# Optimization experiments

Hardware: AMD Instinct MI355X
Metric: run time of the kernel (lower is better)

The kernel has to match this reference:

```python
import jax, jax.numpy as jnp
import numpy as np

DIM = 256
D_STATE = 16
D_CONV = 4
EXPAND = 2
D_INNER = DIM * EXPAND          # 512
DT_RANK = DIM // 16             # 16


def _dwconv(x_bcl, w, b, pad):
    # depthwise 1d conv; x_bcl: (B, C, L), w: (C, 1, K)
    out = jax.lax.conv_general_dilated(
        x_bcl, w, window_strides=(1,), padding=[pad],
        feature_group_count=x_bcl.shape[1],
        dimension_numbers=('NCH', 'OIH', 'NCH'))
    return out + b[None, :, None]


def _forward(x, ln_w, ln_b, W_in, conv_w, conv_b, W_xproj, W_dt, b_dt,
             A_log, D_ssm, W_outp, c1_w, c1_b, c2_w, c2_b, c3_w, c3_b,
             W_out, b_out, W_skip, b_skip):
    Bsz, C = x.shape[:2]
    img_dims = x.shape[2:]
    L = int(np.prod(img_dims))
    xf = x.reshape(Bsz, C, L).transpose(0, 2, 1)          # (B, L, C)
    # LayerNorm over channel dim
    mu = jnp.mean(xf, axis=-1, keepdims=True)
    var = jnp.var(xf, axis=-1, keepdims=True)
    xn = (xf - mu) / jnp.sqrt(var + 1e-5) * ln_w + ln_b   # (B, L, C)

    # ---------------- Mamba block ----------------
    xz = xn @ W_in.T                                      # (B, L, 2*Di)
    xi, z = jnp.split(xz, 2, axis=-1)
    k = conv_w.shape[-1]
    # causal depthwise conv (pad left d_conv-1, truncate to L), then silu
    xc = _dwconv(xi.transpose(0, 2, 1), conv_w, conv_b, (k - 1, 0))
    xc = jax.nn.silu(xc).transpose(0, 2, 1)               # (B, L, Di)
    x_dbl = xc @ W_xproj.T                                # (B, L, dt_rank + 2*N)
    dt = x_dbl[..., :DT_RANK]
    B_s = x_dbl[..., DT_RANK:DT_RANK + D_STATE]           # (B, L, N)
    C_s = x_dbl[..., DT_RANK + D_STATE:]                  # (B, L, N)
    delta = jax.nn.softplus(dt @ W_dt.T + b_dt)           # (B, L, Di)
    A = -jnp.exp(A_log)                                   # (Di, N)
    dA = jnp.exp(delta[..., None] * A)                    # (B, L, Di, N)
    dBu = (delta * xc)[..., None] * B_s[:, :, None, :]    # (B, L, Di, N)

    def step(h, inp):
        dA_t, dBu_t, c_t = inp
        h = dA_t * h + dBu_t                              # (B, Di, N)
        y = jnp.einsum('bdn,bn->bd', h, c_t)
        return h, y

    h0 = jnp.zeros((Bsz, D_INNER, D_STATE), dtype=x.dtype)
    _, ys = jax.lax.scan(
        step, h0,
        (dA.transpose(1, 0, 2, 3), dBu.transpose(1, 0, 2, 3), C_s.transpose(1, 0, 2)))
    y = ys.transpose(1, 0, 2) + D_ssm * xc                # (B, L, Di)
    y = y * jax.nn.silu(z)
    x_ssm = y @ W_outp.T                                  # (B, L, C)

    # ---------------- multi-scale depthwise convs ----------------
    xnT = xn.transpose(0, 2, 1)                           # (B, C, L)

    def msconv(w, b):
        kk = w.shape[-1]
        return jax.nn.silu(_dwconv(xnT, w, b, (kk // 2, kk // 2))).transpose(0, 2, 1)

    combined = x_ssm + msconv(c1_w, c1_b) + msconv(c2_w, c2_b) + msconv(c3_w, c3_b)
    out = combined @ W_out.T + b_out + xn @ W_skip.T + b_skip
    out = out.transpose(0, 2, 1).reshape(x.shape)
    return out + x


def setup_inputs() -> dict:
    key = jax.random.key(0)
    ks = jax.random.split(key, 12)

    def rn(k, shape, s=0.02):
        return jax.random.normal(k, shape, dtype=jnp.float32) * s

    return {
        'x': jax.random.normal(ks[0], (2, DIM, 64, 64), dtype=jnp.float32),
        'ln_w': jnp.ones((DIM,), jnp.float32),
        'ln_b': jnp.zeros((DIM,), jnp.float32),
        'W_in': rn(ks[1], (2 * D_INNER, DIM)),
        'conv_w': rn(ks[2], (D_INNER, 1, D_CONV), 0.1),
        'conv_b': jnp.zeros((D_INNER,), jnp.float32),
        'W_xproj': rn(ks[3], (DT_RANK + 2 * D_STATE, D_INNER)),
        'W_dt': rn(ks[4], (D_INNER, DT_RANK), 0.1),
        'b_dt': jnp.full((D_INNER,), -4.0, jnp.float32),  # softplus(-4) ~ 0.018, stable dt
        'A_log': jnp.log(jnp.broadcast_to(
            jnp.arange(1, D_STATE + 1, dtype=jnp.float32), (D_INNER, D_STATE))),
        'D_ssm': jnp.ones((D_INNER,), jnp.float32),
        'W_outp': rn(ks[5], (DIM, D_INNER)),
        'c1_w': rn(ks[6], (DIM, 1, 3), 0.1),
        'c1_b': jnp.zeros((DIM,), jnp.float32),
        'c2_w': rn(ks[7], (DIM, 1, 5), 0.1),
        'c2_b': jnp.zeros((DIM,), jnp.float32),
        'c3_w': rn(ks[8], (DIM, 1, 7), 0.1),
        'c3_b': jnp.zeros((DIM,), jnp.float32),
        'W_out': rn(ks[9], (DIM, DIM)),
        'b_out': jnp.zeros((DIM,), jnp.float32),
        'W_skip': rn(ks[10], (DIM, DIM)),
        'b_skip': jnp.zeros((DIM,), jnp.float32),
    }


def reference(x, ln_w, ln_b, W_in, conv_w, conv_b, W_xproj, W_dt, b_dt,
              A_log, D_ssm, W_outp, c1_w, c1_b, c2_w, c2_b, c3_w, c3_b,
              W_out, b_out, W_skip, b_skip):
    return _forward(x, ln_w, ln_b, W_in, conv_w, conv_b, W_xproj, W_dt, b_dt,
                    A_log, D_ssm, W_outp, c1_w, c1_b, c2_w, c2_b, c3_w, c3_b,
                    W_out, b_out, W_skip, b_skip)
```

## Files before the change

### kernel.cpp

```cpp
#include <hip/hip_runtime.h>
#include <hip/hip_bf16.h>
#include <math.h>
#include <cstddef>

#define BSZ 2
#define DM 256
#define LSEQ 4096
#define DIN 512
#define DXZ 1024
#define DS 16
#define RANK 16
#define GXP 48
#define LC 16
#define NC 256
#define CSTRIDE (BSZ * DIN * 16)

typedef __attribute__((ext_vector_type(8))) short short8;
typedef __attribute__((ext_vector_type(4))) float f32x4;
struct bf4 { __hip_bfloat16 v[4]; };

__device__ __forceinline__ float silu_f(float x){ return x / (1.f + __expf(-x)); }
__device__ __forceinline__ float softplus_f(float x){ return fmaxf(x, 0.f) + log1pf(__expf(-fabsf(x))); }
__device__ __forceinline__ float b2f(__hip_bfloat16 v){ return __bfloat162float(v); }
__device__ __forceinline__ __hip_bfloat16 f2b(float v){ return __float2bfloat16(v); }

__device__ __forceinline__ void gl_lds16(const void* g, void* s){
    __builtin_amdgcn_global_load_lds((const __attribute__((address_space(1))) void*)g,
                                     (__attribute__((address_space(3))) void*)s, 16, 0, 0);
}

__global__ __launch_bounds__(256) void k_pre(const float* __restrict__ x,
                                             const float* __restrict__ lnw, const float* __restrict__ lnb,
                                             const float* __restrict__ W_in, const float* __restrict__ W_xproj,
                                             const float* __restrict__ W_outp, const float* __restrict__ W_out,
                                             const float* __restrict__ W_skip, const float* __restrict__ b_out,
                                             const float* __restrict__ b_skip, const float* __restrict__ W_dt,
                                             const float* __restrict__ c1w, const float* __restrict__ c1b,
                                             const float* __restrict__ c2w, const float* __restrict__ c2b,
                                             const float* __restrict__ c3w, const float* __restrict__ c3b,
                                             __hip_bfloat16* __restrict__ xnb,
                                             __hip_bfloat16* __restrict__ Winb, __hip_bfloat16* __restrict__ Wxpb,
                                             __hip_bfloat16* __restrict__ Wopb, __hip_bfloat16* __restrict__ Wcb,
                                             __hip_bfloat16* __restrict__ Wdtb, float* __restrict__ bc,
                                             float* __restrict__ msw){
    __shared__ float tile[DM * 33];
    __shared__ float rsum[8][32], rsq[8][32];
    __shared__ float mu_s[32], rs_s[32];
    int tid = threadIdx.x;
    if (blockIdx.x < 256){
        int b  = blockIdx.x >> 7;
        int l0 = (blockIdx.x & 127) << 5;
        const float* xb = x + (size_t)b * DM * LSEQ;
        int lls = tid & 31, chi = tid >> 5;
        for (int cc = 0; cc < 32; ++cc){
            int c = cc * 8 + chi;
            tile[c * 33 + lls] = xb[(size_t)c * LSEQ + l0 + lls];
        }
        __syncthreads();
        int part = tid >> 5, l = tid & 31;
        float s = 0.f, sq = 0.f;
        for (int i = 0; i < 32; ++i){
            float v = tile[(part * 32 + i) * 33 + l];
            s += v; sq += v * v;
        }
        rsum[part][l] = s; rsq[part][l] = sq;
        __syncthreads();
        if (tid < 32){
            float ts = 0.f, tq = 0.f;
            for (int p = 0; p < 8; ++p){ ts += rsum[p][tid]; tq += rsq[p][tid]; }
            float mu  = ts * (1.f / DM);
            float var = tq * (1.f / DM) - mu * mu;
            mu_s[tid] = mu;
            rs_s[tid] = rsqrtf(var + 1e-5f);
        }
        __syncthreads();
        int c0 = tid & 63, lh = tid >> 6;
        for (int i = 0; i < 8; ++i){
            int ll = lh + 4 * i;
            float mu = mu_s[ll], rs = rs_s[ll];
            __hip_bfloat16* orow = xnb + (size_t)(b * LSEQ + l0 + ll) * 512;
            for (int j = 0; j < 4; ++j){
                int c = c0 + 64 * j;
                orow[c] = f2b((tile[c * 33 + ll] - mu) * rs * lnw[c] + lnb[c]);
            }
        }
    } else {
        int i0 = (blockIdx.x - 256) * 256 + tid;
        const int T = 256 * 256;
        for (int j = i0; j < 1024 * 256; j += T) Winb[j] = f2b(W_in[j]);
        for (int j = i0; j < 64 * 512; j += T){
            int r = j >> 9;
            Wxpb[j] = f2b(r < GXP ? W_xproj[r * 512 + (j & 511)] : 0.f);
        }
        for (int j = i0; j < 256 * 512; j += T) Wopb[j] = f2b(W_outp[j]);
        for (int j = i0; j < 256 * 512; j += T){
            int n = j >> 9, k = j & 511;
            Wcb[j] = f2b(k < 256 ? W_out[n * 256 + k] : W_skip[n * 256 + (k - 256)]);
        }
        for (int j = i0; j < 512 * 32; j += T){
            int n = j >> 5, k = j & 31;
            Wdtb[j] = f2b(k < 16 ? W_dt[n * 16 + k] : 0.f);
        }
        if (i0 < 256){
            bc[i0] = b_out[i0] + b_skip[i0];
            float* m = msw + i0 * 20;
            m[0] = c1w[i0*3]; m[1] = c1w[i0*3+1]; m[2] = c1w[i0*3+2];
            for (int j = 0; j < 5; ++j) m[3+j] = c2w[i0*5+j];
            for (int j = 0; j < 7; ++j) m[8+j] = c3w[i0*7+j];
            m[15] = c1b[i0]; m[16] = c2b[i0]; m[17] = c3b[i0];
            m[18] = 0.f; m[19] = 0.f;
        }
    }
}

template<int EPI, int BM = 128, int BN = 64>
__global__ __launch_bounds__(256) void k_mgemm(const __hip_bfloat16* __restrict__ A, int lda,
                                               const __hip_bfloat16* __restrict__ W,
                                               const float* __restrict__ bias,
                                               void* __restrict__ Cv, int ldc,
                                               int N, int K,
                                               const float* __restrict__ xres = nullptr,
                                               const __hip_bfloat16* __restrict__ xnb2 = nullptr,
                                               const float* __restrict__ msw = nullptr){
    constexpr int SA  = BM / 8;
    constexpr int SAW = SA / 4;
    constexpr int SB  = BN / 8;
    constexpr int SBW = SB / 4;
    constexpr int WROWS = BM / 2;
    constexpr int WCOLS = BN / 2;
    constexpr int MI = WROWS / 16;
    constexpr int NI = WCOLS / 16;
    __shared__ __align__(16) __hip_bfloat16 As[BM * 64];
    __shared__ __align__(16) __hip_bfloat16 Ws[BN * 64];
    __shared__ float tileT[(EPI & 16) ? 64 * 65 : 1];
    const int tid = threadIdx.x;
    const int wave = tid >> 6, lane = tid & 63;
    const int brow = blockIdx.x * BM, bcol = blockIdx.y * BN;
    const int wm = wave >> 1, wn = wave & 1;

    const int a_row = lane >> 3;
    const int a_chk = lane & 7;
    const int a_scol = ((a_chk ^ a_row) * 8);

    const int lrow = lane & 15;
    const int kc = lane >> 4;
    const int r7 = lrow & 7;

    f32x4 acc[MI][NI] = {};

    for (int k0 = 0; k0 < K; k0 += 64){
#pragma unroll
        for (int j = 0; j < SAW; ++j){
            int seg = wave * SAW + j;
            const __hip_bfloat16* src = A + (size_t)(brow + seg * 8 + a_row) * lda + k0 + a_scol;
            gl_lds16(src, &As[seg * 512]);
        }
#pragma unroll
        for (int j = 0; j < SBW; ++j){
            int seg = wave * SBW + j;
            const __hip_bfloat16* src = W + (size_t)(bcol + seg * 8 + a_row) * K + k0 + a_scol;
            gl_lds16(src, &Ws[seg * 512]);
        }
        __syncthreads();
#pragma unroll
        for (int kk = 0; kk < 2; ++kk){
            int kchunk = kk * 4 + kc;
            short8 af[MI], bfr[NI];
#pragma unroll
            for (int mi = 0; mi < MI; ++mi){
                int row = wm * WROWS + mi * 16 + lrow;
                af[mi] = *(const short8*)&As[row * 64 + ((kchunk ^ r7) * 8)];
            }
#pragma unroll
            for (int ni = 0; ni < NI; ++ni){
                int row = wn * WCOLS + ni * 16 + lrow;
                bfr[ni] = *(const short8*)&Ws[row * 64 + ((kchunk ^ r7) * 8)];
            }
#pragma unroll
            for (int mi = 0; mi < MI; ++mi)
#pragma unroll
                for (int ni = 0; ni < NI; ++ni)
                    acc[mi][ni] = __builtin_amdgcn_mfma_f32_16x16x32_bf16(af[mi], bfr[ni], acc[mi][ni], 0, 0, 0);
        }
        __syncthreads();
    }

    if (EPI & 16){
#pragma unroll
        for (int ni = 0; ni < NI; ++ni){
            int nl = wn * WCOLS + ni * 16 + lrow;
#pragma unroll
            for (int mi = 0; mi < MI; ++mi){
                int ml = wm * WROWS + mi * 16 + kc * 4;
#pragma unroll
                for (int r = 0; r < 4; ++r)
                    tileT[nl * 65 + ml + r] = acc[mi][ni][r];
            }
        }
        __syncthreads();
        int b = brow >> 12, l0 = brow & 4095;
        int lr = tid & 63, nr = tid >> 6;
        float* out = (float*)Cv;
#pragma unroll
        for (int rr = 0; rr < 16; ++rr){
            int n = rr * 4 + nr;
            size_t o = (size_t)(b * DM + bcol + n) * LSEQ + l0 + lr;
            out[o] = tileT[n * 65 + lr] + bias[bcol + n] + xres[o];
        }
        return;
    }

    if (EPI & 32){
#pragma unroll
        for (int ni = 0; ni < NI; ++ni){
            int n = bcol + wn * WCOLS + ni * 16 + lrow;
            float4 wv0 = *(const float4*)&msw[n * 20];
            float4 wv1 = *(const float4*)&msw[n * 20 + 4];
            float4 wv2 = *(const float4*)&msw[n * 20 + 8];
            float4 wv3 = *(const float4*)&msw[n * 20 + 12];
            float4 wv4 = *(const float4*)&msw[n * 20 + 16];
#pragma unroll
            for (int mi = 0; mi < MI; ++mi){
                int m0 = brow + wm * WROWS + mi * 16 + kc * 4;
                int l  = m0 & (LSEQ - 1);
                int bL = m0 - l;
                float v[10];
#pragma unroll
                for (int k = 0; k < 10; ++k){
                    int ll = l - 3 + k;
                    v[k] = ((unsigned)ll < LSEQ) ? b2f(xnb2[(size_t)(bL + ll) * 512 + n]) : 0.f;
                }
#pragma unroll
                for (int r = 0; r < 4; ++r){
                    float a1 = wv3.w + wv0.x * v[r+2] + wv0.y * v[r+3] + wv0.z * v[r+4];
                    float a2 = wv4.x + wv0.w * v[r+1] + wv1.x * v[r+2] + wv1.y * v[r+3]
                                     + wv1.z * v[r+4] + wv1.w * v[r+5];
                    float a3 = wv4.y + wv2.x * v[r] + wv2.y * v[r+1] + wv2.z * v[r+2]
                                     + wv2.w * v[r+3] + wv3.x * v[r+4] + wv3.y * v[r+5]
                                     + wv3.z * v[r+6];
                    float res = acc[mi][ni][r] + silu_f(a1) + silu_f(a2) + silu_f(a3);
                    ((__hip_bfloat16*)Cv)[(size_t)(m0 + r) * ldc + n] = f2b(res);
                }
            }
        }
        return;
    }

#pragma unroll
    for (int ni = 0; ni < NI; ++ni){
        int n = bcol + wn * WCOLS + ni * 16 + lrow;
        if (n >= N) continue;
        float bv = (EPI & 1) ? bias[n] : 0.f;
#pragma unroll
        for (int mi = 0; mi < MI; ++mi){
            int m0 = brow + wm * WROWS + mi * 16 + kc * 4;
#pragma unroll
            for (int r = 0; r < 4; ++r){
                float v = acc[mi][ni][r] + bv;
                if (EPI & 8) ((__hip_bfloat16*)Cv)[(size_t)(m0 + r) * ldc + n] = f2b(v);
                else         ((float*)Cv)[(size_t)(m0 + r) * ldc + n] = v;
            }
        }
    }
}

__global__ __launch_bounds__(256) void k_xpdt(const __hip_bfloat16* __restrict__ A,
                                              const __hip_bfloat16* __restrict__ Wxp,
                                              const __hip_bfloat16* __restrict__ Wdt,
                                              const float* __restrict__ bdt,
                                              float* __restrict__ xdbl,
                                              __hip_bfloat16* __restrict__ delta){
    __shared__ __align__(16) __hip_bfloat16 As[32 * 64];
    __shared__ __align__(16) __hip_bfloat16 Ws[64 * 64];
    __shared__ __hip_bfloat16 xdl[32][34];
    const int tid = threadIdx.x, wave = tid >> 6, lane = tid & 63;
    const int brow = blockIdx.x * 32;
    const int wm = wave >> 1, wn = wave & 1;
    const int a_row = lane >> 3, a_chk = lane & 7, a_scol = ((a_chk ^ a_row) * 8);
    const int lrow = lane & 15, kc = lane >> 4, r7 = lrow & 7;

    for (int i = tid; i < 32 * 18; i += 256){
        int rr = i / 18, cc = 16 + i % 18;
        xdl[rr][cc] = f2b(0.f);
    }

    f32x4 acc[2] = {};
    for (int k0 = 0; k0 < 512; k0 += 64){
        {
            int seg = wave;
            gl_lds16(A + (size_t)(brow + seg * 8 + a_row) * 512 + k0 + a_scol, &As[seg * 512]);
        }
#pragma unroll
        for (int j = 0; j < 2; ++j){
            int seg = wave * 2 + j;
            gl_lds16(Wxp + (size_t)(seg * 8 + a_row) * 512 + k0 + a_scol, &Ws[seg * 512]);
        }
        __syncthreads();
#pragma unroll
        for (int kk = 0; kk < 2; ++kk){
            int kchunk = kk * 4 + kc;
            short8 af = *(const short8*)&As[(wm * 16 + lrow) * 64 + ((kchunk ^ r7) * 8)];
#pragma unroll
            for (int ni = 0; ni < 2; ++ni){
                short8 bfr = *(const short8*)&Ws[(wn * 32 + ni * 16 + lrow) * 64 + ((kchunk ^ r7) * 8)];
                acc[ni] = __builtin_amdgcn_mfma_f32_16x16x32_bf16(af, bfr, acc[ni], 0, 0, 0);
            }
        }
        __syncthreads();
    }

#pragma unroll
    for (int ni = 0; ni < 2; ++ni){
        int n = wn * 32 + ni * 16 + lrow;
        if (n < 48){
#pragma unroll
            for (int r = 0; r < 4; ++r){
                int ml = wm * 16 + kc * 4 + r;
                float fv = acc[ni][r];
                xdbl[(size_t)(brow + ml) * 48 + n] = fv;
                if (n < 16) xdl[ml][n] = f2b(fv);
            }
        }
    }
    __syncthreads();

#pragma unroll
    for (int ct8 = 0; ct8 < 8; ++ct8){
        int ct = wave * 8 + ct8;
        int n = ct * 16 + lrow;
        short8 bfr = *(const short8*)&Wdt[(size_t)n * 32 + kc * 8];
        float bv = bdt[n];
#pragma unroll
        for (int rt = 0; rt < 2; ++rt){
            short8 af = *(const short8*)&xdl[rt * 16 + lrow][kc * 8];
            f32x4 dacc = {};
            dacc = __builtin_amdgcn_mfma_f32_16x16x32_bf16(af, bfr, dacc, 0, 0, 0);
#pragma unroll
            for (int r = 0; r < 4; ++r){
                int m = brow + rt * 16 + kc * 4 + r;
                delta[(size_t)m * 512 + n] = f2b(softplus_f(dacc[r] + bv));
            }
        }
    }
}

__global__ __launch_bounds__(256) void k_conv(const __hip_bfloat16* __restrict__ xz,
                                              const float* __restrict__ cw,
                                              const float* __restrict__ cb,
                                              __hip_bfloat16* __restrict__ xc){
    int idx = blockIdx.x * 256 + threadIdx.x;
    int d4 = (idx & 127) * 4;
    int bl = idx >> 7;
    int l  = bl & (LSEQ - 1);
    const __hip_bfloat16* base = xz + (size_t)bl * DXZ + d4;
    float4 bias = *(const float4*)(cb + d4);
    float acc[4] = {bias.x, bias.y, bias.z, bias.w};
    float4 w0 = *(const float4*)(cw + (d4 + 0) * 4);
    float4 w1 = *(const float4*)(cw + (d4 + 1) * 4);
    float4 w2 = *(const float4*)(cw + (d4 + 2) * 4);
    float4 w3 = *(const float4*)(cw + (d4 + 3) * 4);
    const float* wj[4] = {(const float*)&w0, (const float*)&w1, (const float*)&w2, (const float*)&w3};
#pragma unroll
    for (int t = 0; t < 4; ++t){
        int ls = l - (3 - t);
        if (ls >= 0){
            bf4 v = *(const bf4*)(base - (size_t)(3 - t) * DXZ);
#pragma unroll
            for (int j = 0; j < 4; ++j) acc[j] += wj[j][t] * b2f(v.v[j]);
        }
    }
    bf4 o;
#pragma unroll
    for (int j = 0; j < 4; ++j) o.v[j] = f2b(silu_f(acc[j]));
    *(bf4*)(xc + (size_t)bl * DIN + d4) = o;
}

__global__ __launch_bounds__(512) void k_scan1(const __hip_bfloat16* __restrict__ delta,
                                               const __hip_bfloat16* __restrict__ xc,
                                               const float* __restrict__ xdbl,
                                               const float* __restrict__ A_log,
                                               float* __restrict__ Acar,
                                               float* __restrict__ Bcar){
    int bx = blockIdx.x;
    int dh = bx & 1;
    int c  = (bx >> 1) & (NC - 1);
    int b  = bx >> 9;
    int tid = threadIdx.x;
    int dloc = tid >> 1, nh = tid & 1;
    int d = dh * 256 + dloc;
    int n0 = nh * 8;
    int rb = b * LSEQ + c * LC;
    __shared__ __align__(16) __hip_bfloat16 dl[LC][256];
    __shared__ __align__(16) __hip_bfloat16 xl[LC][256];
    __shared__ float Bs[LC][DS];
    const int w = tid >> 6, lane = tid & 63;
    {
        size_t rowg = (size_t)(rb + 2 * w + (lane >> 5));
        int col = (lane & 31) * 8;
        gl_lds16(delta + rowg * 512 + dh * 256 + col, &dl[2 * w][0]);
        gl_lds16(xc    + rowg * 512 + dh * 256 + col, &xl[2 * w][0]);
    }
    if (tid < 256){
        int t = tid >> 4, n = tid & 15;
        Bs[t][n] = xdbl[(size_t)(rb + t) * GXP + RANK + n];
    }
    __syncthreads();
    float Av[8];
    float a1 = -__expf(A_log[d * 16]);
    bool fast = true;
#pragma unroll
    for (int j = 0; j < 8; ++j){
        Av[j] = -__expf(A_log[d * 16 + n0 + j]);
        fast = fast && (fabsf(Av[j] - (float)(n0 + j + 1) * a1) <= 1e-4f * fabsf(Av[j]) + 1e-7f);
    }
    float ap[8], ac[8];
#pragma unroll
    for (int j = 0; j < 8; ++j){ ap[j] = 1.f; ac[j] = 0.f; }
    if (fast){
#pragma unroll 4
        for (int t = 0; t < LC; ++t){
            float de = b2f(dl[t][dloc]);
            float u  = de * b2f(xl[t][dloc]);
            float p  = __expf(de * a1);
            float p2 = p * p, p3 = p2 * p, p4 = p2 * p2;
            float qda[8] = {p, p2, p3, p4, p4 * p, p4 * p2, p4 * p3, p4 * p4};
            float bp = nh ? qda[7] : 1.f;
#pragma unroll
            for (int j = 0; j < 8; ++j){
                float da = qda[j] * bp;
                ap[j] *= da;
                ac[j] = da * ac[j] + u * Bs[t][n0 + j];
            }
        }
    } else {
        for (int t = 0; t < LC; ++t){
            float de = b2f(dl[t][dloc]);
            float u  = de * b2f(xl[t][dloc]);
#pragma unroll
            for (int j = 0; j < 8; ++j){
                float da = __expf(de * Av[j]);
                ap[j] *= da;
                ac[j] = da * ac[j] + u * Bs[t][n0 + j];
            }
        }
    }
    size_t o = (size_t)c * CSTRIDE + (size_t)(b * DIN + d) * 16 + n0;
    *(float4*)(Acar + o)     = make_float4(ap[0], ap[1], ap[2], ap[3]);
    *(float4*)(Acar + o + 4) = make_float4(ap[4], ap[5], ap[6], ap[7]);
    *(float4*)(Bcar + o)     = make_float4(ac[0], ac[1], ac[2], ac[3]);
    *(float4*)(Bcar + o + 4) = make_float4(ac[4], ac[5], ac[6], ac[7]);
}

__global__ __launch_bounds__(256) void k_scan2(const float* __restrict__ Acar,
                                               const float* __restrict__ Bcar,
                                               float* __restrict__ hinit){
    __shared__ float a_s[16][257];
    __shared__ float b_s[16][257];
    const int tid = threadIdx.x;
    const int idx0 = blockIdx.x * 16;
    const int cs = tid >> 4, s_ld = tid & 15;
#pragma unroll
    for (int r = 0; r < 16; ++r){
        int c = r * 16 + cs;
        size_t g = (size_t)c * CSTRIDE + idx0 + s_ld;
        a_s[s_ld][c] = Acar[g];
        b_s[s_ld][c] = Bcar[g];
    }
    __syncthreads();
    const int lane = tid & 63, w = tid >> 6;
#pragma unroll
    for (int i = 0; i < 4; ++i){
        int s = w * 4 + i;
        float a4[4], b4[4];
#pragma unroll
        for (int k = 0; k < 4; ++k){ a4[k] = a_s[s][4 * lane + k]; b4[k] = b_s[s][4 * lane + k]; }
        float av = a4[0], bv = b4[0];
#pragma unroll
        for (int k = 1; k < 4; ++k){ bv = a4[k] * bv + b4[k]; av *= a4[k]; }
#pragma unroll
        for (int d2 = 1; d2 < 64; d2 <<= 1){
            float ao = __shfl_up(av, d2);
            float bo = __shfl_up(bv, d2);
            if (lane >= d2){ bv = av * bo + bv; av = ao * av; }
        }
        float bx = __shfl_up(bv, 1);
        if (lane == 0) bx = 0.f;
        float h = bx;
        b_s[s][4 * lane] = h;
#pragma unroll
        for (int k = 0; k < 3; ++k){ h = a4[k] * h + b4[k]; b_s[s][4 * lane + 1 + k] = h; }
    }
    __syncthreads();
#pragma unroll
    for (int r = 0; r < 16; ++r){
        int c = r * 16 + cs;
        hinit[(size_t)c * CSTRIDE + idx0 + s_ld] = b_s[s_ld][c];
    }
}

__global__ __launch_bounds__(512) void k_scan3(const __hip_bfloat16* __restrict__ delta,
                                               const __hip_bfloat16* __restrict__ xc,
                                               const __hip_bfloat16* __restrict__ xz,
                                               const float* __restrict__ xdbl,
                                               const float* __restrict__ A_log,
                                               const float* __restrict__ D_ssm,
                                               const float* __restrict__ hinit,
                                               __hip_bfloat16* __restrict__ y){
    int bx = blockIdx.x;
    int dh = bx & 1;
    int c  = (bx >> 1) & (NC - 1);
    int b  = bx >> 9;
    int tid = threadIdx.x;
    int dloc = tid >> 1, nh = tid & 1;
    int d = dh * 256 + dloc;
    int n0 = nh * 8;
    int rb = b * LSEQ + c * LC;
    __shared__ __align__(16) __hip_bfloat16 dl[LC][256];
    __shared__ __align__(16) __hip_bfloat16 xl[LC][256];
    __shared__ __align__(16) __hip_bfloat16 zl[LC][256];
    __shared__ float Bs[LC][DS], Cs[LC][DS];
    const int w = tid >> 6, lane = tid & 63;
    {
        size_t rowg = (size_t)(rb + 2 * w + (lane >> 5));
        int col = (lane & 31) * 8;
        gl_lds16(delta + rowg * 512 + dh * 256 + col, &dl[2 * w][0]);
        gl_lds16(xc    + rowg * 512 + dh * 256 + col, &xl[2 * w][0]);
        gl_lds16(xz    + rowg * 1024 + 512 + dh * 256 + col, &zl[2 * w][0]);
    }
    if (tid < 256){
        int t = tid >> 4, n = tid & 15;
        Bs[t][n] = xdbl[(size_t)(rb + t) * GXP + RANK + n];
    } else {
        int t = (tid >> 4) - 16, n = tid & 15;
        Cs[t][n] = xdbl[(size_t)(rb + t) * GXP + RANK + DS + n];
    }
    __syncthreads();
    float Av[8];
    float a1 = -__expf(A_log[d * 16]);
    bool fast = true;
#pragma unroll
    for (int j = 0; j < 8; ++j){
        Av[j] = -__expf(A_log[d * 16 + n0 + j]);
        fast = fast && (fabsf(Av[j] - (float)(n0 + j + 1) * a1) <= 1e-4f * fabsf(Av[j]) + 1e-7f);
    }
    float h[8];
    size_t ho = (size_t)c * CSTRIDE + (size_t)(b * DIN + d) * 16 + n0;
    {
        float4 h0 = *(const float4*)(hinit + ho);
        float4 h1 = *(const float4*)(hinit + ho + 4);
        h[0] = h0.x; h[1] = h0.y; h[2] = h0.z; h[3] = h0.w;
        h[4] = h1.x; h[5] = h1.y; h[6] = h1.z; h[7] = h1.w;
    }
    float Dd = D_ssm[d];
    if (fast){
#pragma unroll 4
        for (int t = 0; t < LC; ++t){
            float de  = b2f(dl[t][dloc]);
            float xcv = b2f(xl[t][dloc]);
            float u = de * xcv;
            float p  = __expf(de * a1);
            float p2 = p * p, p3 = p2 * p, p4 = p2 * p2;
            float qda[8] = {p, p2, p3, p4, p4 * p, p4 * p2, p4 * p3, p4 * p4};
            float bp = nh ? qda[7] : 1.f;
#pragma unroll
            for (int j = 0; j < 8; ++j)
                h[j] = (qda[j] * bp) * h[j] + u * Bs[t][n0 + j];
            float e0 = h[0] * Cs[t][n0]     + h[1] * Cs[t][n0 + 1];
            float e1 = h[2] * Cs[t][n0 + 2] + h[3] * Cs[t][n0 + 3];
            float e2 = h[4] * Cs[t][n0 + 4] + h[5] * Cs[t][n0 + 5];
            float e3 = h[6] * Cs[t][n0 + 6] + h[7] * Cs[t][n0 + 7];
            float yv = (e0 + e1) + (e2 + e3);
            yv += __shfl_xor(yv, 1);
            if (nh == 0){
                float zv = b2f(zl[t][dloc]);
                zl[t][dloc] = f2b((yv + Dd * xcv) * silu_f(zv));
            }
        }
    } else {
        for (int t = 0; t < LC; ++t){
            float de  = b2f(dl[t][dloc]);
            float xcv = b2f(xl[t][dloc]);
            float u = de * xcv;
            float yv = 0.f;
#pragma unroll
            for (int j = 0; j < 8; ++j){
                float da = __expf(de * Av[j]);
                h[j] = da * h[j] + u * Bs[t][n0 + j];
                yv += h[j] * Cs[t][n0 + j];
            }
            yv += __shfl_xor(yv, 1);
            if (nh == 0){
                float zv = b2f(zl[t][dloc]);
                zl[t][dloc] = f2b((yv + Dd * xcv) * silu_f(zv));
            }
        }
    }
    __syncthreads();
    {
        int row = tid >> 5, colv = (tid & 31) * 8;
        *(float4*)(y + (size_t)(rb + row) * 512 + dh * 256 + colv) = *(const float4*)(&zl[row][colv]);
    }
}

extern "C" void kernel_launch(void* const* d_in, const int* in_sizes, int n_in,
                              void* d_out, int out_size, void* d_ws, size_t ws_size,
                              hipStream_t stream){
    const float* x      = (const float*)d_in[0];
    const float* ln_w   = (const float*)d_in[1];
    const float* ln_b   = (const float*)d_in[2];
    const float* W_in   = (const float*)d_in[3];
    const float* conv_w = (const float*)d_in[4];
    const float* conv_b = (const float*)d_in[5];
    const float* W_xproj= (const float*)d_in[6];
    const float* W_dt   = (const float*)d_in[7];
    const float* b_dt   = (const float*)d_in[8];
    const float* A_log  = (const float*)d_in[9];
    const float* D_ssm  = (const float*)d_in[10];
    const float* W_outp = (const float*)d_in[11];
    const float* c1_w   = (const float*)d_in[12];
    const float* c1_b   = (const float*)d_in[13];
    const float* c2_w   = (const float*)d_in[14];
    const float* c2_b   = (const float*)d_in[15];
    const float* c3_w   = (const float*)d_in[16];
    const float* c3_b   = (const float*)d_in[17];
    const float* W_out  = (const float*)d_in[18];
    const float* b_out  = (const float*)d_in[19];
    const float* W_skip = (const float*)d_in[20];
    const float* b_skip = (const float*)d_in[21];
    float* out = (float*)d_out;

    char* base = (char*)d_ws;
    const size_t MB = 1024 * 1024;
    const size_t KB = 1024;
    __hip_bfloat16* Acomb = (__hip_bfloat16*)(base);
    __hip_bfloat16* xzb   = (__hip_bfloat16*)(base + 8*MB);
    __hip_bfloat16* xcb   = (__hip_bfloat16*)(base + 24*MB);
    float*          xdbl  = (float*)        (base + 32*MB);
    __hip_bfloat16* deltab= (__hip_bfloat16*)(base + 34*MB);
    float*          Acar  = (float*)        (base + 42*MB);
    float*          Bcar  = (float*)        (base + 58*MB);
    float*          hinit = (float*)        (base + 74*MB);
    __hip_bfloat16* Winb  = (__hip_bfloat16*)(base + 90*MB);
    __hip_bfloat16* Wxpb  = (__hip_bfloat16*)(base + 90*MB + 512*KB);
    __hip_bfloat16* Wopb  = (__hip_bfloat16*)(base + 90*MB + 576*KB);
    __hip_bfloat16* Wcb   = (__hip_bfloat16*)(base + 90*MB + 832*KB);
    __hip_bfloat16* Wdtb  = (__hip_bfloat16*)(base + 90*MB + 1088*KB);
    float*          bc    = (float*)        (base + 90*MB + 1120*KB);
    float*          msw   = (float*)        (base + 90*MB + 1124*KB);
    __hip_bfloat16* xnb   = Acomb + 256;
    __hip_bfloat16* ybf   = (__hip_bfloat16*)Bcar;

    const int M = BSZ * LSEQ;

    k_pre<<<dim3(512), dim3(256), 0, stream>>>(x, ln_w, ln_b, W_in, W_xproj, W_outp, W_out, W_skip,
                                               b_out, b_skip, W_dt, c1_w, c1_b, c2_w, c2_b, c3_w, c3_b,
                                               xnb, Winb, Wxpb, Wopb, Wcb, Wdtb, bc, msw);
    k_mgemm<8, 128, 128><<<dim3(64, 8), dim3(256), 0, stream>>>(xnb, 512, Winb, nullptr, xzb, DXZ, 1024, 256);
    k_conv<<<dim3(M * DIN / 4 / 256), dim3(256), 0, stream>>>(xzb, conv_w, conv_b, xcb);
    k_xpdt<<<dim3(256), dim3(256), 0, stream>>>(xcb, Wxpb, Wdtb, b_dt, xdbl, deltab);
    k_scan1<<<dim3(BSZ * NC * 2), dim3(512), 0, stream>>>(deltab, xcb, xdbl, A_log, Acar, Bcar);
    k_scan2<<<dim3(1024), dim3(256), 0, stream>>>(Acar, Bcar, hinit);
    k_scan3<<<dim3(BSZ * NC * 2), dim3(512), 0, stream>>>(deltab, xcb, xzb, xdbl, A_log, D_ssm, hinit, ybf);
    k_mgemm<32, 64, 64><<<dim3(128, 4), dim3(256), 0, stream>>>(ybf, 512, Wopb, nullptr, Acomb, 512, 256, 512,
                                                                nullptr, xnb, msw);
    k_mgemm<17, 64, 64><<<dim3(128, 4), dim3(256), 0, stream>>>(Acomb, 512, Wcb, bc, out, DM, 256, 512, x);
}
```

Baseline: 233.9 us.

## Fuse chunk-scan pass 1 into x-proj/delta kernel and store carries in bf16

```diff
diff --git a/kernel.cpp b/kernel.cpp
--- a/kernel.cpp
+++ b/kernel.cpp
@@ -268,11 +268,16 @@
                                               const __hip_bfloat16* __restrict__ Wxp,
                                               const __hip_bfloat16* __restrict__ Wdt,
                                               const float* __restrict__ bdt,
+                                              const float* __restrict__ A_log,
                                               float* __restrict__ xdbl,
-                                              __hip_bfloat16* __restrict__ delta){
+                                              __hip_bfloat16* __restrict__ delta,
+                                              __hip_bfloat16* __restrict__ Acar,
+                                              __hip_bfloat16* __restrict__ Bcar){
     __shared__ __align__(16) __hip_bfloat16 As[32 * 64];
     __shared__ __align__(16) __hip_bfloat16 Ws[64 * 64];
     __shared__ __hip_bfloat16 xdl[32][34];
+    __shared__ __hip_bfloat16 dls[32][520];
+    __shared__ float Bls[32][16];
     const int tid = threadIdx.x, wave = tid >> 6, lane = tid & 63;
     const int brow = blockIdx.x * 32;
     const int wm = wave >> 1, wn = wave & 1;
@@ -319,6 +324,7 @@
                 float fv = acc[ni][r];
                 xdbl[(size_t)(brow + ml) * 48 + n] = fv;
                 if (n < 16) xdl[ml][n] = f2b(fv);
+                else if (n < 32) Bls[ml][n - 16] = fv;
             }
         }
     }
@@ -337,9 +343,71 @@
             dacc = __builtin_amdgcn_mfma_f32_16x16x32_bf16(af, bfr, dacc, 0, 0, 0);
 #pragma unroll
             for (int r = 0; r < 4; ++r){
-                int m = brow + rt * 16 + kc * 4 + r;
-                delta[(size_t)m * 512 + n] = f2b(softplus_f(dacc[r] + bv));
-            }
+                int ml = rt * 16 + kc * 4 + r;
+                __hip_bfloat16 hv = f2b(softplus_f(dacc[r] + bv));
+                delta[(size_t)(brow + ml) * 512 + n] = hv;
+                dls[ml][n] = hv;
+            }
+        }
+    }
+    __syncthreads();
+
+    const int b = brow >> 12;
+    const int c0 = (brow & 4095) >> 4;
+#pragma unroll
+    for (int dd = 0; dd < 2; ++dd){
+        int d = dd * 256 + tid;
+        float a1 = -__expf(A_log[d * 16]);
+        float Av[16];
+        bool fast = true;
+#pragma unroll
+        for (int j = 0; j < 16; ++j){
+            Av[j] = -__expf(A_log[d * 16 + j]);
+            fast = fast && (fabsf(Av[j] - (float)(j + 1) * a1) <= 1e-4f * fabsf(Av[j]) + 1e-7f);
+        }
+#pragma unroll
+        for (int cc = 0; cc < 2; ++cc){
+            float ap[16], ac[16];
+#pragma unroll
+            for (int j = 0; j < 16; ++j){ ap[j] = 1.f; ac[j] = 0.f; }
+            if (fast){
+                for (int t = 0; t < LC; ++t){
+                    int ml = cc * 16 + t;
+                    float de = b2f(dls[ml][d]);
+                    float u  = de * b2f(A[(size_t)(brow + ml) * 512 + d]);
+                    float p  = __expf(de * a1);
+                    float q2 = p * p;
+                    float q3 = q2 * p, q4 = q2 * q2;
+                    float q5 = q4 * p, q6 = q4 * q2, q7 = q4 * q3, q8 = q4 * q4;
+                    float qa[16] = {p, q2, q3, q4, q5, q6, q7, q8,
+                                    q8 * p, q8 * q2, q8 * q3, q8 * q4, q8 * q5, q8 * q6, q8 * q7, q8 * q8};
+#pragma unroll
+                    for (int j = 0; j < 16; ++j){
+                        ap[j] *= qa[j];
+                        ac[j] = qa[j] * ac[j] + u * Bls[ml][j];
+                    }
+                }
+            } else {
+                for (int t = 0; t < LC; ++t){
+                    int ml = cc * 16 + t;
+                    float de = b2f(dls[ml][d]);
+                    float u  = de * b2f(A[(size_t)(brow + ml) * 512 + d]);
+#pragma unroll
+                    for (int j = 0; j < 16; ++j){
+                        float da = __expf(de * Av[j]);
+                        ap[j] *= da;
+                        ac[j] = da * ac[j] + u * Bls[ml][j];
+                    }
+                }
+            }
+            __hip_bfloat16 av16[16], bv16[16];
+#pragma unroll
+            for (int j = 0; j < 16; ++j){ av16[j] = f2b(ap[j]); bv16[j] = f2b(ac[j]); }
+            size_t o = (size_t)(c0 + cc) * CSTRIDE + (size_t)(b * DIN + d) * 16;
+            *(float4*)(Acar + o)     = *(const float4*)(av16);
+            *(float4*)(Acar + o + 8) = *(const float4*)(av16 + 8);
+            *(float4*)(Bcar + o)     = *(const float4*)(bv16);
+            *(float4*)(Bcar + o + 8) = *(const float4*)(bv16 + 8);
         }
     }
 }
@@ -375,85 +443,9 @@
     *(bf4*)(xc + (size_t)bl * DIN + d4) = o;
 }
 
-__global__ __launch_bounds__(512) void k_scan1(const __hip_bfloat16* __restrict__ delta,
-                                               const __hip_bfloat16* __restrict__ xc,
-                                               const float* __restrict__ xdbl,
-                                               const float* __restrict__ A_log,
-                                               float* __restrict__ Acar,
-                                               float* __restrict__ Bcar){
-    int bx = blockIdx.x;
-    int dh = bx & 1;
-    int c  = (bx >> 1) & (NC - 1);
-    int b  = bx >> 9;
-    int tid = threadIdx.x;
-    int dloc = tid >> 1, nh = tid & 1;
-    int d = dh * 256 + dloc;
-    int n0 = nh * 8;
-    int rb = b * LSEQ + c * LC;
-    __shared__ __align__(16) __hip_bfloat16 dl[LC][256];
-    __shared__ __align__(16) __hip_bfloat16 xl[LC][256];
-    __shared__ float Bs[LC][DS];
-    const int w = tid >> 6, lane = tid & 63;
-    {
-        size_t rowg = (size_t)(rb + 2 * w + (lane >> 5));
-        int col = (lane & 31) * 8;
-        gl_lds16(delta + rowg * 512 + dh * 256 + col, &dl[2 * w][0]);
-        gl_lds16(xc    + rowg * 512 + dh * 256 + col, &xl[2 * w][0]);
-    }
-    if (tid < 256){
-        int t = tid >> 4, n = tid & 15;
-        Bs[t][n] = xdbl[(size_t)(rb + t) * GXP + RANK + n];
-    }
-    __syncthreads();
-    float Av[8];
-    float a1 = -__expf(A_log[d * 16]);
-    bool fast = true;
-#pragma unroll
-    for (int j = 0; j < 8; ++j){
-        Av[j] = -__expf(A_log[d * 16 + n0 + j]);
-        fast = fast && (fabsf(Av[j] - (float)(n0 + j + 1) * a1) <= 1e-4f * fabsf(Av[j]) + 1e-7f);
-    }
-    float ap[8], ac[8];
-#pragma unroll
-    for (int j = 0; j < 8; ++j){ ap[j] = 1.f; ac[j] = 0.f; }
-    if (fast){
-#pragma unroll 4
-        for (int t = 0; t < LC; ++t){
-            float de = b2f(dl[t][dloc]);
-            float u  = de * b2f(xl[t][dloc]);
-            float p  = __expf(de * a1);
-            float p2 = p * p, p3 = p2 * p, p4 = p2 * p2;
-            float qda[8] = {p, p2, p3, p4, p4 * p, p4 * p2, p4 * p3, p4 * p4};
-            float bp = nh ? qda[7] : 1.f;
-#pragma unroll
-            for (int j = 0; j < 8; ++j){
-                float da = qda[j] * bp;
-                ap[j] *= da;
-                ac[j] = da * ac[j] + u * Bs[t][n0 + j];
-            }
-        }
-    } else {
-        for (int t = 0; t < LC; ++t){
-            float de = b2f(dl[t][dloc]);
-            float u  = de * b2f(xl[t][dloc]);
-#pragma unroll
-            for (int j = 0; j < 8; ++j){
-                float da = __expf(de * Av[j]);
-                ap[j] *= da;
-                ac[j] = da * ac[j] + u * Bs[t][n0 + j];
-            }
-        }
-    }
-    size_t o = (size_t)c * CSTRIDE + (size_t)(b * DIN + d) * 16 + n0;
-    *(float4*)(Acar + o)     = make_float4(ap[0], ap[1], ap[2], ap[3]);
-    *(float4*)(Acar + o + 4) = make_float4(ap[4], ap[5], ap[6], ap[7]);
-    *(float4*)(Bcar + o)     = make_float4(ac[0], ac[1], ac[2], ac[3]);
-    *(float4*)(Bcar + o + 4) = make_float4(ac[4], ac[5], ac[6], ac[7]);
-}
-
-__global__ __launch_bounds__(256) void k_scan2(const float* __restrict__ Acar,
-                                               const float* __restrict__ Bcar,
-                                               float* __restrict__ hinit){
+__global__ __launch_bounds__(256) void k_scan2(const __hip_bfloat16* __restrict__ Acar,
+                                               const __hip_bfloat16* __restrict__ Bcar,
+                                               __hip_bfloat16* __restrict__ hinit){
     __shared__ float a_s[16][257];
     __shared__ float b_s[16][257];
     const int tid = threadIdx.x;
@@ -463,8 +455,8 @@
     for (int r = 0; r < 16; ++r){
         int c = r * 16 + cs;
         size_t g = (size_t)c * CSTRIDE + idx0 + s_ld;
-        a_s[s_ld][c] = Acar[g];
-        b_s[s_ld][c] = Bcar[g];
+        a_s[s_ld][c] = b2f(Acar[g]);
+        b_s[s_ld][c] = b2f(Bcar[g]);
     }
     __syncthreads();
     const int lane = tid & 63, w = tid >> 6;
@@ -494,7 +486,7 @@
 #pragma unroll
     for (int r = 0; r < 16; ++r){
         int c = r * 16 + cs;
-        hinit[(size_t)c * CSTRIDE + idx0 + s_ld] = b_s[s_ld][c];
+        hinit[(size_t)c * CSTRIDE + idx0 + s_ld] = f2b(b_s[s_ld][c]);
     }
 }
 
@@ -504,7 +496,7 @@
                                                const float* __restrict__ xdbl,
                                                const float* __restrict__ A_log,
                                                const float* __restrict__ D_ssm,
-                                               const float* __restrict__ hinit,
+                                               const __hip_bfloat16* __restrict__ hinit,
                                                __hip_bfloat16* __restrict__ y){
     int bx = blockIdx.x;
     int dh = bx & 1;
@@ -546,10 +538,9 @@
     float h[8];
     size_t ho = (size_t)c * CSTRIDE + (size_t)(b * DIN + d) * 16 + n0;
     {
-        float4 h0 = *(const float4*)(hinit + ho);
-        float4 h1 = *(const float4*)(hinit + ho + 4);
-        h[0] = h0.x; h[1] = h0.y; h[2] = h0.z; h[3] = h0.w;
-        h[4] = h1.x; h[5] = h1.y; h[6] = h1.z; h[7] = h1.w;
+        short8 hv = *(const short8*)(hinit + ho);
+#pragma unroll
+        for (int j = 0; j < 8; ++j) h[j] = b2f(((const __hip_bfloat16*)&hv)[j]);
     }
     float Dd = D_ssm[d];
     if (fast){
@@ -637,18 +628,18 @@
     __hip_bfloat16* xcb   = (__hip_bfloat16*)(base + 24*MB);
     float*          xdbl  = (float*)        (base + 32*MB);
     __hip_bfloat16* deltab= (__hip_bfloat16*)(base + 34*MB);
-    float*          Acar  = (float*)        (base + 42*MB);
-    float*          Bcar  = (float*)        (base + 58*MB);
-    float*          hinit = (float*)        (base + 74*MB);
-    __hip_bfloat16* Winb  = (__hip_bfloat16*)(base + 90*MB);
-    __hip_bfloat16* Wxpb  = (__hip_bfloat16*)(base + 90*MB + 512*KB);
-    __hip_bfloat16* Wopb  = (__hip_bfloat16*)(base + 90*MB + 576*KB);
-    __hip_bfloat16* Wcb   = (__hip_bfloat16*)(base + 90*MB + 832*KB);
-    __hip_bfloat16* Wdtb  = (__hip_bfloat16*)(base + 90*MB + 1088*KB);
-    float*          bc    = (float*)        (base + 90*MB + 1120*KB);
-    float*          msw   = (float*)        (base + 90*MB + 1124*KB);
+    __hip_bfloat16* Acar  = (__hip_bfloat16*)(base + 42*MB);
+    __hip_bfloat16* Bcar  = (__hip_bfloat16*)(base + 50*MB);
+    __hip_bfloat16* hinit = (__hip_bfloat16*)(base + 58*MB);
+    __hip_bfloat16* Winb  = (__hip_bfloat16*)(base + 66*MB);
+    __hip_bfloat16* Wxpb  = (__hip_bfloat16*)(base + 66*MB + 512*KB);
+    __hip_bfloat16* Wopb  = (__hip_bfloat16*)(base + 66*MB + 576*KB);
+    __hip_bfloat16* Wcb   = (__hip_bfloat16*)(base + 66*MB + 832*KB);
+    __hip_bfloat16* Wdtb  = (__hip_bfloat16*)(base + 66*MB + 1088*KB);
+    float*          bc    = (float*)        (base + 66*MB + 1120*KB);
+    float*          msw   = (float*)        (base + 66*MB + 1124*KB);
     __hip_bfloat16* xnb   = Acomb + 256;
-    __hip_bfloat16* ybf   = (__hip_bfloat16*)Bcar;
+    __hip_bfloat16* ybf   = Bcar;
 
     const int M = BSZ * LSEQ;
 
@@ -657,8 +648,7 @@
                                                xnb, Winb, Wxpb, Wopb, Wcb, Wdtb, bc, msw);
     k_mgemm<8, 128, 128><<<dim3(64, 8), dim3(256), 0, stream>>>(xnb, 512, Winb, nullptr, xzb, DXZ, 1024, 256);
     k_conv<<<dim3(M * DIN / 4 / 256), dim3(256), 0, stream>>>(xzb, conv_w, conv_b, xcb);
-    k_xpdt<<<dim3(256), dim3(256), 0, stream>>>(xcb, Wxpb, Wdtb, b_dt, xdbl, deltab);
-    k_scan1<<<dim3(BSZ * NC * 2), dim3(512), 0, stream>>>(deltab, xcb, xdbl, A_log, Acar, Bcar);
+    k_xpdt<<<dim3(256), dim3(256), 0, stream>>>(xcb, Wxpb, Wdtb, b_dt, A_log, xdbl, deltab, Acar, Bcar);
     k_scan2<<<dim3(1024), dim3(256), 0, stream>>>(Acar, Bcar, hinit);
     k_scan3<<<dim3(BSZ * NC * 2), dim3(512), 0, stream>>>(deltab, xcb, xzb, xdbl, A_log, D_ssm, hinit, ybf);
     k_mgemm<32, 64, 64><<<dim3(128, 4), dim3(256), 0, stream>>>(ybf, 512, Wopb, nullptr, Acomb, 512, 256, 512,
```

Measured after the change: 229.3 us. 2.0% less time.
